# Performance work log

Measured on AMD Instinct MI355X. Metric: run time of the kernel, lower is better.

The kernel has to match this reference:

```python
import jax, jax.numpy as jnp
import numpy as np

B_IN, C, K, P, STRIDE, ITERS = 32, 32, 3, 4, 2, 3
PSIZE = P * P


def _patch(t):
    # t: (b, h, w, B, d) -> (b, oh, ow, K, K, B, d), matching torch fancy-index patching
    b, h, w = t.shape[:3]
    oh = int((h - K + 1) / STRIDE)
    idx = (np.arange(oh) * STRIDE)[:, None] + np.arange(K)[None, :]  # (oh, K)
    t = t[:, idx]          # (b, oh, K, w, B, d)
    t = t[:, :, :, idx]    # (b, oh, K, ow, K, B, d)
    perm = (0, 1, 3, 2, 4) + tuple(range(5, t.ndim))
    return jnp.transpose(t, perm), oh, oh


def _forward(x, a, weights, beta_u, beta_a):
    b = x.shape[0]
    KKB = K * K * B_IN
    p_in, oh, ow = _patch(x)
    a_in, _, _ = _patch(a)
    pose = p_in.reshape(b, oh, ow, KKB, P, P)
    a_in = a_in.reshape(b, oh, ow, KKB, 1)
    # voting: per-capsule 4x4 matmul with transformation matrices
    v = jnp.einsum('bhwnij,ncjl->bhwncil', pose, weights).reshape(b, oh, ow, KKB, C, PSIZE)
    eps = 1e-6
    lam = 1e-3
    ln2pi = np.float32(np.log(2.0 * np.pi))
    mu = sigma_sq = a_out = None
    for it in range(ITERS):
        if it == 0:
            r = jnp.full((b, oh, ow, KKB, C), 1.0 / C, jnp.float32) * a_in  # a_in broadcasts over C
        else:
            # gaussian log-likelihood of each vote under each output capsule
            ln_pjh = -(v - mu) ** 2 / (2.0 * sigma_sq) - 0.5 * jnp.log(sigma_sq) - 0.5 * ln2pi
            ln_ap = ln_pjh.sum(axis=5) + jnp.log(a_out.reshape(b, oh, ow, 1, C))
            r = jax.nn.softmax(ln_ap, axis=4)
        r_sum = r.sum(axis=3, keepdims=True)               # (b,oh,ow,1,C)
        coeff = (r / (r_sum + eps))[..., None]             # (b,oh,ow,KKB,C,1)
        mu = (coeff * v).sum(axis=3, keepdims=True)        # (b,oh,ow,1,C,PSIZE)
        sigma_sq = (coeff * (v - mu) ** 2).sum(axis=3, keepdims=True) + eps
        # beta_u: (C,1) broadcasts against (...,C,PSIZE); log(sqrt(s)) == 0.5*log(s)
        cost_h = (beta_u + 0.5 * jnp.log(sigma_sq)) * r_sum[..., None]
        a_out = jax.nn.sigmoid(lam * (beta_a - cost_h.sum(axis=5, keepdims=True)))
    p_out = mu.reshape(b, oh, ow, C, PSIZE)
    a_out = a_out.reshape(b, oh, ow, C, 1)
    return p_out, a_out


def setup_inputs() -> dict:
    key = jax.random.key(0)
    k1, k2, k3, k4, k5 = jax.random.split(key, 5)
    x = jax.random.normal(k1, (8, 14, 14, B_IN, PSIZE), jnp.float32)
    a = jax.random.uniform(k2, (8, 14, 14, B_IN, 1), jnp.float32)
    weights = jax.random.normal(k3, (K * K * B_IN, C, P, P), jnp.float32)
    beta_u = jax.random.normal(k4, (C, 1), jnp.float32) * 0.1
    beta_a = jax.random.normal(k5, (C, 1), jnp.float32) * 0.1
    return {"x": x, "a": a, "weights": weights, "beta_u": beta_u, "beta_a": beta_a}


def reference(x, a, weights, beta_u, beta_a):
    return _forward(x, a, weights, beta_u, beta_a)
```

## Files before the change

kernel.cpp:

```cpp
#include <hip/hip_runtime.h>

#define APB 256
#define NPOS 288
#define NCH 6
#define CHUNK 48
#define PSTRIDE 1056


template<int IT>
__global__ __launch_bounds__(APB) void caps_acc(
    const float* __restrict__ xg,
    const float* __restrict__ ag,
    const float* __restrict__ wg,
    const float* __restrict__ bu,
    const float* __restrict__ ba,
    const float* __restrict__ pin,
    float* __restrict__ pout)
{
    __shared__ __align__(16) float pose_s[CHUNK * 16];
    __shared__ float a_s[CHUNK];
    __shared__ __align__(16) float scratch[4 * 32 * 33];
    __shared__ float rsum_part[4 * 32];
    __shared__ float mu_tab[512];
    __shared__ float i2s_tab[512];
    __shared__ float Kc_tab[32];

    const int tid = threadIdx.x;
    const int blk = blockIdx.x;
    const int pos = blk / NCH;
    const int ch  = blk - pos * NCH;
    const int bb  = pos / 36;
    const int rem = pos % 36;
    const int yy  = rem / 6;
    const int xx  = rem % 6;

    #pragma unroll
    for (int j = 0; j < 3; ++j) {
        const int e    = ch * 768 + j * 256 + tid;
        const int cell = e >> 9;
        const int off  = e & 511;
        const int kh = cell / 3, kw = cell % 3;
        pose_s[j * 256 + tid] =
            xg[(size_t)((((bb * 14) + (2 * yy + kh)) * 14 + (2 * xx + kw)) * 32) * 16 + off];
    }
    if (IT == 0) {
        if (tid < CHUNK) {
            const int e    = ch * CHUNK + tid;
            const int cell = e >> 5;
            const int bi   = e & 31;
            const int kh = cell / 3, kw = cell % 3;
            a_s[tid] = ag[(size_t)(((bb * 14) + (2 * yy + kh)) * 14 + (2 * xx + kw)) * 32 + bi];
        }
    }

    const int fc2 = tid >> 3;
    const int fh  = tid & 7;
    if (IT > 0) {
        const float* q0 = pin + (size_t)pos * (NCH * PSTRIDE) + fc2 * 33;
        float ms0 = 0.f, ms1 = 0.f, vs0 = 0.f, vs1 = 0.f, rsc = 0.f;
        #pragma unroll
        for (int cc = 0; cc < NCH; ++cc) {
            const float* q = q0 + cc * PSTRIDE;
            ms0 += q[fh];
            ms1 += q[fh + 8];
            vs0 += q[16 + fh];
            vs1 += q[16 + fh + 8];
            rsc += q[32];
        }
        const float inv  = 1.f / (rsc + 1e-6f);
        const float S    = rsc * inv;
        const float mu0  = ms0 * inv;
        const float mu1  = ms1 * inv;
        const float sig0 = vs0 * inv - mu0 * mu0 * (2.f - S) + 1e-6f;
        const float sig1 = vs1 * inv - mu1 * mu1 * (2.f - S) + 1e-6f;
        float lgs = __logf(sig0) + __logf(sig1);
        #pragma unroll
        for (int msk = 4; msk >= 1; msk >>= 1) lgs += __shfl_xor(lgs, msk);
        const float cost = rsc * (16.f * bu[fc2] + 0.5f * lgs);
        const float ao   = 1.f / (1.f + __expf(-0.001f * (ba[fc2] - cost)));
        mu_tab[fc2 * 16 + fh]      = mu0;
        mu_tab[fc2 * 16 + fh + 8]  = mu1;
        i2s_tab[fc2 * 16 + fh]     = 0.5f / sig0;
        i2s_tab[fc2 * 16 + fh + 8] = 0.5f / sig1;
        if (fh == 0) Kc_tab[fc2] = 0.5f * lgs - __logf(ao);
    }
    __syncthreads();

    const int c    = tid & 31;
    const int s    = tid >> 5;
    const int lane = tid & 63;
    const int wv   = tid >> 6;
    const float4* wp = (const float4*)wg;

    float mu_c[16], i2s_c[16], Kc = 0.f;
    if (IT > 0) {
        #pragma unroll
        for (int p = 0; p < 16; ++p) {
            mu_c[p]  = mu_tab[c * 16 + p];
            i2s_c[p] = i2s_tab[c * 16 + p];
        }
        Kc = Kc_tab[c];
    }
    float macc[16], vacc[16], rs = 0.f;
    #pragma unroll
    for (int p = 0; p < 16; ++p) { macc[p] = 0.f; vacc[p] = 0.f; }

    for (int k = 0; k < 6; ++k) {
        const int nl = s * 6 + k;
        const int n  = ch * CHUNK + nl;
        const float4* pp = (const float4*)&pose_s[nl << 4];
        float pf[16];
        float4 q;
        q = pp[0]; pf[0]=q.x;  pf[1]=q.y;  pf[2]=q.z;  pf[3]=q.w;
        q = pp[1]; pf[4]=q.x;  pf[5]=q.y;  pf[6]=q.z;  pf[7]=q.w;
        q = pp[2]; pf[8]=q.x;  pf[9]=q.y;  pf[10]=q.z; pf[11]=q.w;
        q = pp[3]; pf[12]=q.x; pf[13]=q.y; pf[14]=q.z; pf[15]=q.w;
        const int wbase = (n * 32 + c) * 4;
        float v[16];
        #pragma unroll
        for (int p = 0; p < 16; ++p) v[p] = 0.f;
        #pragma unroll
        for (int j = 0; j < 4; ++j) {
            const float4 w = wp[wbase + j];
            #pragma unroll
            for (int i = 0; i < 4; ++i) {
                const float pj = pf[i * 4 + j];
                v[i*4+0] = fmaf(pj, w.x, v[i*4+0]);
                v[i*4+1] = fmaf(pj, w.y, v[i*4+1]);
                v[i*4+2] = fmaf(pj, w.z, v[i*4+2]);
                v[i*4+3] = fmaf(pj, w.w, v[i*4+3]);
            }
        }
        float r;
        if (IT == 0) {
            r = a_s[nl] * 0.03125f;
        } else {
            float t0 = 0.f, t1 = 0.f, t2 = 0.f, t3 = 0.f;
            #pragma unroll
            for (int p = 0; p < 16; p += 4) {
                float d0 = v[p]   - mu_c[p];   t0 = fmaf(d0*d0, i2s_c[p],   t0);
                float d1 = v[p+1] - mu_c[p+1]; t1 = fmaf(d1*d1, i2s_c[p+1], t1);
                float d2 = v[p+2] - mu_c[p+2]; t2 = fmaf(d2*d2, i2s_c[p+2], t2);
                float d3 = v[p+3] - mu_c[p+3]; t3 = fmaf(d3*d3, i2s_c[p+3], t3);
            }
            float lnap = -((t0 + t1) + (t2 + t3)) - Kc;
            float m = lnap;
            #pragma unroll
            for (int msk = 16; msk >= 1; msk >>= 1) m = fmaxf(m, __shfl_xor(m, msk));
            float e = __expf(lnap - m);
            float sum = e;
            #pragma unroll
            for (int msk = 16; msk >= 1; msk >>= 1) sum += __shfl_xor(sum, msk);
            r = e / sum;
        }
        rs += r;
        #pragma unroll
        for (int p = 0; p < 16; ++p) {
            float rv = r * v[p];
            macc[p] += rv;
            vacc[p] = fmaf(rv, v[p], vacc[p]);
        }
    }

    #pragma unroll
    for (int p = 0; p < 16; ++p) {
        macc[p] += __shfl_xor(macc[p], 32);
        vacc[p] += __shfl_xor(vacc[p], 32);
    }
    rs += __shfl_xor(rs, 32);
    if (lane < 32) {
        const int base = (wv * 32 + lane) * 33;
        #pragma unroll
        for (int p = 0; p < 16; ++p) {
            scratch[base + p]      = macc[p];
            scratch[base + 16 + p] = vacc[p];
        }
        rsum_part[wv * 32 + lane] = rs;
    }
    __syncthreads();

    float ms0 = 0.f, ms1 = 0.f, vs0 = 0.f, vs1 = 0.f, rsc = 0.f;
    #pragma unroll
    for (int w = 0; w < 4; ++w) {
        const int base = (w * 32 + fc2) * 33;
        ms0 += scratch[base + fh];
        ms1 += scratch[base + fh + 8];
        vs0 += scratch[base + 16 + fh];
        vs1 += scratch[base + 16 + fh + 8];
        rsc += rsum_part[w * 32 + fc2];
    }
    float* po = pout + (size_t)(pos * NCH + ch) * PSTRIDE + fc2 * 33;
    po[fh]          = ms0;
    po[fh + 8]      = ms1;
    po[16 + fh]     = vs0;
    po[16 + fh + 8] = vs1;
    if (fh == 0) po[32] = rsc;
}

__global__ __launch_bounds__(512) void caps_fin(
    const float* __restrict__ pin,
    const float* __restrict__ bu,
    const float* __restrict__ ba,
    float* __restrict__ outp)
{
    const int tid = threadIdx.x;
    const int pos = blockIdx.x;
    const int fc = tid >> 4, fp = tid & 15;
    const float* q0 = pin + (size_t)pos * (NCH * PSTRIDE) + fc * 33;
    float ms = 0.f, vs = 0.f, rsc = 0.f;
    #pragma unroll
    for (int cc = 0; cc < NCH; ++cc) {
        const float* q = q0 + cc * PSTRIDE;
        ms  += q[fp];
        vs  += q[16 + fp];
        rsc += q[32];
    }
    const float inv = 1.f / (rsc + 1e-6f);
    const float S   = rsc * inv;
    const float mu  = ms * inv;
    const float sig = vs * inv - mu * mu * (2.f - S) + 1e-6f;
    const float lg  = __logf(sig);
    float lgs = lg;
    #pragma unroll
    for (int msk = 8; msk >= 1; msk >>= 1) lgs += __shfl_xor(lgs, msk);
    const float cost = rsc * (16.f * bu[fc] + 0.5f * lgs);
    const float ao   = 1.f / (1.f + __expf(-0.001f * (ba[fc] - cost)));
    outp[(size_t)pos * 512 + tid] = mu;
    if (fp == 0) outp[147456 + (size_t)pos * 32 + fc] = ao;
}

__global__ __launch_bounds__(512) void convcaps_kernel(
    const float* __restrict__ xg,
    const float* __restrict__ ag,
    const float* __restrict__ wg,
    const float* __restrict__ bu,
    const float* __restrict__ ba,
    float* __restrict__ outp)
{
    __shared__ __align__(16) float pose_s[4608];
    __shared__ float a_s[288];
    __shared__ __align__(16) float scratch[8448];
    __shared__ float rsum_part[256];
    __shared__ float mu_tab[512];
    __shared__ float i2s_tab[512];
    __shared__ float aout_tab[32];
    __shared__ float Kc_tab[32];

    const int tid = threadIdx.x;
    const int pos = blockIdx.x;
    const int bb  = pos / 36;
    const int rem = pos % 36;
    const int yy  = rem / 6;
    const int xx  = rem % 6;

    #pragma unroll
    for (int wi = 0; wi < 9; ++wi) {
        const int kh = wi / 3, kw = wi % 3;
        const float* src =
            xg + (size_t)((((bb * 14) + (2 * yy + kh)) * 14 + (2 * xx + kw)) * 32) * 16;
        pose_s[wi * 512 + tid] = src[tid];
    }
    if (tid < 288) {
        const int wi = tid >> 5, bi = tid & 31;
        const int kh = wi / 3, kw = wi % 3;
        a_s[tid] = ag[(size_t)(((bb * 14) + (2 * yy + kh)) * 14 + (2 * xx + kw)) * 32 + bi];
    }
    __syncthreads();

    const int c    = tid & 31;
    const int s    = tid >> 5;
    const int lane = tid & 63;
    const int wv   = tid >> 6;
    const float4* wp = (const float4*)wg;

    for (int it = 0; it < 3; ++it) {
        float mu_c[16], i2s_c[16], Kc = 0.f;
        if (it > 0) {
            #pragma unroll
            for (int p = 0; p < 16; ++p) {
                mu_c[p]  = mu_tab[c * 16 + p];
                i2s_c[p] = i2s_tab[c * 16 + p];
            }
            Kc = Kc_tab[c];
        }
        float macc[16], vacc[16], rs = 0.f;
        #pragma unroll
        for (int p = 0; p < 16; ++p) { macc[p] = 0.f; vacc[p] = 0.f; }

        for (int k = 0; k < 18; ++k) {
            const int n = s * 18 + k;
            const float4* pp = (const float4*)&pose_s[n << 4];
            float pf[16];
            float4 q;
            q = pp[0]; pf[0]=q.x; pf[1]=q.y; pf[2]=q.z;  pf[3]=q.w;
            q = pp[1]; pf[4]=q.x; pf[5]=q.y; pf[6]=q.z;  pf[7]=q.w;
            q = pp[2]; pf[8]=q.x; pf[9]=q.y; pf[10]=q.z; pf[11]=q.w;
            q = pp[3]; pf[12]=q.x; pf[13]=q.y; pf[14]=q.z; pf[15]=q.w;
            const int wbase = (n * 32 + c) * 4;
            float v[16];
            #pragma unroll
            for (int p = 0; p < 16; ++p) v[p] = 0.f;
            #pragma unroll
            for (int j = 0; j < 4; ++j) {
                const float4 w = wp[wbase + j];
                #pragma unroll
                for (int i = 0; i < 4; ++i) {
                    const float pj = pf[i * 4 + j];
                    v[i*4+0] = fmaf(pj, w.x, v[i*4+0]);
                    v[i*4+1] = fmaf(pj, w.y, v[i*4+1]);
                    v[i*4+2] = fmaf(pj, w.z, v[i*4+2]);
                    v[i*4+3] = fmaf(pj, w.w, v[i*4+3]);
                }
            }
            float r;
            if (it == 0) {
                r = a_s[n] * 0.03125f;
            } else {
                float t = 0.f;
                #pragma unroll
                for (int p = 0; p < 16; ++p) {
                    float d = v[p] - mu_c[p];
                    t = fmaf(d * d, i2s_c[p], t);
                }
                float lnap = -t - Kc;
                float m = lnap;
                #pragma unroll
                for (int msk = 16; msk >= 1; msk >>= 1) m = fmaxf(m, __shfl_xor(m, msk));
                float e = __expf(lnap - m);
                float sum = e;
                #pragma unroll
                for (int msk = 16; msk >= 1; msk >>= 1) sum += __shfl_xor(sum, msk);
                r = e / sum;
            }
            rs += r;
            #pragma unroll
            for (int p = 0; p < 16; ++p) {
                float rv = r * v[p];
                macc[p] += rv;
                vacc[p] = fmaf(rv, v[p], vacc[p]);
            }
        }

        #pragma unroll
        for (int p = 0; p < 16; ++p) {
            macc[p] += __shfl_xor(macc[p], 32);
            vacc[p] += __shfl_xor(vacc[p], 32);
        }
        rs += __shfl_xor(rs, 32);
        if (lane < 32) {
            const int base = (wv * 32 + lane) * 33;
            #pragma unroll
            for (int p = 0; p < 16; ++p) {
                scratch[base + p]      = macc[p];
                scratch[base + 16 + p] = vacc[p];
            }
            rsum_part[wv * 32 + lane] = rs;
        }
        __syncthreads();

        const int fc = tid >> 4, fp = tid & 15;
        float ms = 0.f, vs = 0.f, rsc = 0.f;
        #pragma unroll
        for (int w = 0; w < 8; ++w) {
            ms  += scratch[(w * 32 + fc) * 33 + fp];
            vs  += scratch[(w * 32 + fc) * 33 + 16 + fp];
            rsc += rsum_part[w * 32 + fc];
        }
        const float inv = 1.f / (rsc + 1e-6f);
        const float S   = rsc * inv;
        const float mu  = ms * inv;
        const float sig = vs * inv - mu * mu * (2.f - S) + 1e-6f;
        const float lg  = __logf(sig);
        float lgs = lg;
        #pragma unroll
        for (int msk = 8; msk >= 1; msk >>= 1) lgs += __shfl_xor(lgs, msk);
        const float buv  = bu[fc];
        const float bav  = ba[fc];
        const float cost = rsc * (16.f * buv + 0.5f * lgs);
        const float ao   = 1.f / (1.f + __expf(-0.001f * (bav - cost)));

        mu_tab[fc * 16 + fp]  = mu;
        i2s_tab[fc * 16 + fp] = 0.5f / sig;
        if (fp == 0) {
            aout_tab[fc] = ao;
            Kc_tab[fc]   = 0.5f * lgs - __logf(ao);
        }

        if (it == 2) {
            outp[(size_t)pos * 512 + tid] = mu;
            if (fp == 0) outp[147456 + (size_t)pos * 32 + fc] = ao;
        }
        __syncthreads();
    }
}

extern "C" void kernel_launch(void* const* d_in, const int* in_sizes, int n_in,
                              void* d_out, int out_size, void* d_ws, size_t ws_size,
                              hipStream_t stream) {
    (void)in_sizes; (void)n_in; (void)out_size;
    const float* x  = (const float*)d_in[0];
    const float* a  = (const float*)d_in[1];
    const float* w  = (const float*)d_in[2];
    const float* bu = (const float*)d_in[3];
    const float* ba = (const float*)d_in[4];
    float* out = (float*)d_out;

    const size_t buf_elems = (size_t)NPOS * NCH * PSTRIDE;
    if (ws_size < 2 * buf_elems * sizeof(float)) {
        convcaps_kernel<<<dim3(288), dim3(512), 0, stream>>>(x, a, w, bu, ba, out);
        return;
    }
    float* buf0 = (float*)d_ws;
    float* buf1 = buf0 + buf_elems;

    caps_acc<0><<<dim3(NPOS * NCH), dim3(APB), 0, stream>>>(x, a, w, bu, ba, nullptr, buf0);
    caps_acc<1><<<dim3(NPOS * NCH), dim3(APB), 0, stream>>>(x, a, w, bu, ba, buf0, buf1);
    caps_acc<2><<<dim3(NPOS * NCH), dim3(APB), 0, stream>>>(x, a, w, bu, ba, buf1, buf0);
    caps_fin<<<dim3(NPOS), dim3(512), 0, stream>>>(buf0, bu, ba, out);
}
```

Baseline: 142.5 us.

## Fuse final reduction into last EM pass and streamline E-step math

Removes the separate finalize kernel by having the last of the six chunk blocks per position, found through an atomic counter, compute mu and the activations. It expands the Gaussian exponent into precomputed a·v², b·v and constant tables, and uses DPP lane moves for the 32-lane softmax reductions. It also prefetches the next weight matrix in registers, pads the per-capsule partial layout so loads and stores are float4, and uses a fast divide. The counter fusion adds threadfence and atomic overhead, and the algebraic expansion may lose some precision.

```diff
diff --git a/kernel.cpp b/kernel.cpp
--- a/kernel.cpp
+++ b/kernel.cpp
@@ -1,29 +1,84 @@
 #include <hip/hip_runtime.h>
 
-#define APB 256
 #define NPOS 288
 #define NCH 6
 #define CHUNK 48
-#define PSTRIDE 1056
-
+#define CSTRIDE 36
+#define PSTRIDE (32 * CSTRIDE)
+
+template<int CTRL>
+__device__ __forceinline__ float dpp_mov(float x) {
+    return __int_as_float(__builtin_amdgcn_update_dpp(
+        0, __float_as_int(x), CTRL, 0xF, 0xF, true));
+}
+__device__ __forceinline__ float red32_max(float x) {
+    x = fmaxf(x, dpp_mov<0x121>(x));
+    x = fmaxf(x, dpp_mov<0x122>(x));
+    x = fmaxf(x, dpp_mov<0x124>(x));
+    x = fmaxf(x, dpp_mov<0x128>(x));
+    return fmaxf(x, __shfl_xor(x, 16));
+}
+__device__ __forceinline__ float red32_sum(float x) {
+    x += dpp_mov<0x121>(x);
+    x += dpp_mov<0x122>(x);
+    x += dpp_mov<0x124>(x);
+    x += dpp_mov<0x128>(x);
+    return x + __shfl_xor(x, 16);
+}
+
+#define DOT4(pa, c0, c1, c2, c3) fmaf(pa.x, c0, fmaf(pa.y, c1, fmaf(pa.z, c2, pa.w * c3)))
+#define VROWS() \
+    v0.x = DOT4(pa0, wa0.x, wa1.x, wa2.x, wa3.x); \
+    v0.y = DOT4(pa0, wa0.y, wa1.y, wa2.y, wa3.y); \
+    v0.z = DOT4(pa0, wa0.z, wa1.z, wa2.z, wa3.z); \
+    v0.w = DOT4(pa0, wa0.w, wa1.w, wa2.w, wa3.w); \
+    v1.x = DOT4(pa1, wa0.x, wa1.x, wa2.x, wa3.x); \
+    v1.y = DOT4(pa1, wa0.y, wa1.y, wa2.y, wa3.y); \
+    v1.z = DOT4(pa1, wa0.z, wa1.z, wa2.z, wa3.z); \
+    v1.w = DOT4(pa1, wa0.w, wa1.w, wa2.w, wa3.w); \
+    v2.x = DOT4(pa2, wa0.x, wa1.x, wa2.x, wa3.x); \
+    v2.y = DOT4(pa2, wa0.y, wa1.y, wa2.y, wa3.y); \
+    v2.z = DOT4(pa2, wa0.z, wa1.z, wa2.z, wa3.z); \
+    v2.w = DOT4(pa2, wa0.w, wa1.w, wa2.w, wa3.w); \
+    v3.x = DOT4(pa3, wa0.x, wa1.x, wa2.x, wa3.x); \
+    v3.y = DOT4(pa3, wa0.y, wa1.y, wa2.y, wa3.y); \
+    v3.z = DOT4(pa3, wa0.z, wa1.z, wa2.z, wa3.z); \
+    v3.w = DOT4(pa3, wa0.w, wa1.w, wa2.w, wa3.w);
+#define SQ4(d, v) d.x = v.x*v.x; d.y = v.y*v.y; d.z = v.z*v.z; d.w = v.w*v.w;
+#define TU4(t, u, v, q, A, B) \
+    t = fmaf(q.x, A.x, t); u = fmaf(v.x, B.x, u); \
+    t = fmaf(q.y, A.y, t); u = fmaf(v.y, B.y, u); \
+    t = fmaf(q.z, A.z, t); u = fmaf(v.z, B.z, u); \
+    t = fmaf(q.w, A.w, t); u = fmaf(v.w, B.w, u);
+#define RACC(mai, vai, vi, qi) \
+    mai.x = fmaf(r, vi.x, mai.x); vai.x = fmaf(r, qi.x, vai.x); \
+    mai.y = fmaf(r, vi.y, mai.y); vai.y = fmaf(r, qi.y, vai.y); \
+    mai.z = fmaf(r, vi.z, mai.z); vai.z = fmaf(r, qi.z, vai.z); \
+    mai.w = fmaf(r, vi.w, mai.w); vai.w = fmaf(r, qi.w, vai.w);
+#define XRED(vi) \
+    vi.x += __shfl_xor(vi.x, 32); vi.y += __shfl_xor(vi.y, 32); \
+    vi.z += __shfl_xor(vi.z, 32); vi.w += __shfl_xor(vi.w, 32);
 
 template<int IT>
-__global__ __launch_bounds__(APB) void caps_acc(
+__global__ __launch_bounds__(256) void caps_acc(
     const float* __restrict__ xg,
     const float* __restrict__ ag,
     const float* __restrict__ wg,
     const float* __restrict__ bu,
     const float* __restrict__ ba,
     const float* __restrict__ pin,
-    float* __restrict__ pout)
+    float* __restrict__ pout,
+    float* __restrict__ outg,
+    unsigned* __restrict__ cnt)
 {
     __shared__ __align__(16) float pose_s[CHUNK * 16];
     __shared__ float a_s[CHUNK];
     __shared__ __align__(16) float scratch[4 * 32 * 33];
     __shared__ float rsum_part[4 * 32];
-    __shared__ float mu_tab[512];
     __shared__ float i2s_tab[512];
-    __shared__ float Kc_tab[32];
+    __shared__ float b_tab[512];
+    __shared__ float c_tab[32];
+    __shared__ int   last_s;
 
     const int tid = threadIdx.x;
     const int blk = blockIdx.x;
@@ -51,38 +106,43 @@
             const int kh = cell / 3, kw = cell % 3;
             a_s[tid] = ag[(size_t)(((bb * 14) + (2 * yy + kh)) * 14 + (2 * xx + kw)) * 32 + bi];
         }
+        if (ch == 0 && tid == 0) cnt[pos] = 0u;
     }
 
     const int fc2 = tid >> 3;
     const int fh  = tid & 7;
     if (IT > 0) {
-        const float* q0 = pin + (size_t)pos * (NCH * PSTRIDE) + fc2 * 33;
+        const float* q0 = pin + (size_t)pos * (NCH * PSTRIDE) + fc2 * CSTRIDE;
         float ms0 = 0.f, ms1 = 0.f, vs0 = 0.f, vs1 = 0.f, rsc = 0.f;
         #pragma unroll
         for (int cc = 0; cc < NCH; ++cc) {
             const float* q = q0 + cc * PSTRIDE;
-            ms0 += q[fh];
-            ms1 += q[fh + 8];
-            vs0 += q[16 + fh];
-            vs1 += q[16 + fh + 8];
+            const float4 m4 = *(const float4*)&q[fh * 4];
+            ms0 += m4.x; ms1 += m4.y; vs0 += m4.z; vs1 += m4.w;
             rsc += q[32];
         }
         const float inv  = 1.f / (rsc + 1e-6f);
         const float S    = rsc * inv;
-        const float mu0  = ms0 * inv;
-        const float mu1  = ms1 * inv;
-        const float sig0 = vs0 * inv - mu0 * mu0 * (2.f - S) + 1e-6f;
-        const float sig1 = vs1 * inv - mu1 * mu1 * (2.f - S) + 1e-6f;
-        float lgs = __logf(sig0) + __logf(sig1);
-        #pragma unroll
-        for (int msk = 4; msk >= 1; msk >>= 1) lgs += __shfl_xor(lgs, msk);
+        const float mmu0 = ms0 * inv;
+        const float mmu1 = ms1 * inv;
+        const float sg0  = vs0 * inv - mmu0 * mmu0 * (2.f - S) + 1e-6f;
+        const float sg1  = vs1 * inv - mmu1 * mmu1 * (2.f - S) + 1e-6f;
+        const float i0   = 0.5f / sg0;
+        const float i1   = 0.5f / sg1;
+        float lgs = __logf(sg0) + __logf(sg1);
+        float m2  = fmaf(mmu0 * mmu0, i0, mmu1 * mmu1 * i1);
+        #pragma unroll
+        for (int msk = 4; msk >= 1; msk >>= 1) {
+            lgs += __shfl_xor(lgs, msk);
+            m2  += __shfl_xor(m2, msk);
+        }
         const float cost = rsc * (16.f * bu[fc2] + 0.5f * lgs);
         const float ao   = 1.f / (1.f + __expf(-0.001f * (ba[fc2] - cost)));
-        mu_tab[fc2 * 16 + fh]      = mu0;
-        mu_tab[fc2 * 16 + fh + 8]  = mu1;
-        i2s_tab[fc2 * 16 + fh]     = 0.5f / sig0;
-        i2s_tab[fc2 * 16 + fh + 8] = 0.5f / sig1;
-        if (fh == 0) Kc_tab[fc2] = 0.5f * lgs - __logf(ao);
+        i2s_tab[fc2 * 16 + fh]     = i0;
+        i2s_tab[fc2 * 16 + fh + 8] = i1;
+        b_tab[fc2 * 16 + fh]       = mmu0 * i0;
+        b_tab[fc2 * 16 + fh + 8]   = mmu1 * i1;
+        if (fh == 0) c_tab[fc2] = m2 + 0.5f * lgs - __logf(ao);
     }
     __syncthreads();
 
@@ -92,89 +152,81 @@
     const int wv   = tid >> 6;
     const float4* wp = (const float4*)wg;
 
-    float mu_c[16], i2s_c[16], Kc = 0.f;
+    float4 A0, A1, A2, A3, B0, B1, B2, B3;
+    float C = 0.f;
     if (IT > 0) {
-        #pragma unroll
-        for (int p = 0; p < 16; ++p) {
-            mu_c[p]  = mu_tab[c * 16 + p];
-            i2s_c[p] = i2s_tab[c * 16 + p];
-        }
-        Kc = Kc_tab[c];
-    }
-    float macc[16], vacc[16], rs = 0.f;
-    #pragma unroll
-    for (int p = 0; p < 16; ++p) { macc[p] = 0.f; vacc[p] = 0.f; }
-
-    for (int k = 0; k < 6; ++k) {
-        const int nl = s * 6 + k;
-        const int n  = ch * CHUNK + nl;
-        const float4* pp = (const float4*)&pose_s[nl << 4];
-        float pf[16];
-        float4 q;
-        q = pp[0]; pf[0]=q.x;  pf[1]=q.y;  pf[2]=q.z;  pf[3]=q.w;
-        q = pp[1]; pf[4]=q.x;  pf[5]=q.y;  pf[6]=q.z;  pf[7]=q.w;
-        q = pp[2]; pf[8]=q.x;  pf[9]=q.y;  pf[10]=q.z; pf[11]=q.w;
-        q = pp[3]; pf[12]=q.x; pf[13]=q.y; pf[14]=q.z; pf[15]=q.w;
-        const int wbase = (n * 32 + c) * 4;
-        float v[16];
-        #pragma unroll
-        for (int p = 0; p < 16; ++p) v[p] = 0.f;
-        #pragma unroll
-        for (int j = 0; j < 4; ++j) {
-            const float4 w = wp[wbase + j];
-            #pragma unroll
-            for (int i = 0; i < 4; ++i) {
-                const float pj = pf[i * 4 + j];
-                v[i*4+0] = fmaf(pj, w.x, v[i*4+0]);
-                v[i*4+1] = fmaf(pj, w.y, v[i*4+1]);
-                v[i*4+2] = fmaf(pj, w.z, v[i*4+2]);
-                v[i*4+3] = fmaf(pj, w.w, v[i*4+3]);
-            }
-        }
-        float r;
-        if (IT == 0) {
-            r = a_s[nl] * 0.03125f;
-        } else {
-            float t0 = 0.f, t1 = 0.f, t2 = 0.f, t3 = 0.f;
-            #pragma unroll
-            for (int p = 0; p < 16; p += 4) {
-                float d0 = v[p]   - mu_c[p];   t0 = fmaf(d0*d0, i2s_c[p],   t0);
-                float d1 = v[p+1] - mu_c[p+1]; t1 = fmaf(d1*d1, i2s_c[p+1], t1);
-                float d2 = v[p+2] - mu_c[p+2]; t2 = fmaf(d2*d2, i2s_c[p+2], t2);
-                float d3 = v[p+3] - mu_c[p+3]; t3 = fmaf(d3*d3, i2s_c[p+3], t3);
-            }
-            float lnap = -((t0 + t1) + (t2 + t3)) - Kc;
-            float m = lnap;
-            #pragma unroll
-            for (int msk = 16; msk >= 1; msk >>= 1) m = fmaxf(m, __shfl_xor(m, msk));
-            float e = __expf(lnap - m);
-            float sum = e;
-            #pragma unroll
-            for (int msk = 16; msk >= 1; msk >>= 1) sum += __shfl_xor(sum, msk);
-            r = e / sum;
-        }
-        rs += r;
-        #pragma unroll
-        for (int p = 0; p < 16; ++p) {
-            float rv = r * v[p];
-            macc[p] += rv;
-            vacc[p] = fmaf(rv, v[p], vacc[p]);
-        }
-    }
-
-    #pragma unroll
-    for (int p = 0; p < 16; ++p) {
-        macc[p] += __shfl_xor(macc[p], 32);
-        vacc[p] += __shfl_xor(vacc[p], 32);
-    }
+        A0 = *(const float4*)&i2s_tab[c * 16 + 0];
+        A1 = *(const float4*)&i2s_tab[c * 16 + 4];
+        A2 = *(const float4*)&i2s_tab[c * 16 + 8];
+        A3 = *(const float4*)&i2s_tab[c * 16 + 12];
+        B0 = *(const float4*)&b_tab[c * 16 + 0];
+        B1 = *(const float4*)&b_tab[c * 16 + 4];
+        B2 = *(const float4*)&b_tab[c * 16 + 8];
+        B3 = *(const float4*)&b_tab[c * 16 + 12];
+        C  = c_tab[c];
+    }
+
+    float4 ma0, ma1, ma2, ma3, va0, va1, va2, va3;
+    ma0 = ma1 = ma2 = ma3 = make_float4(0.f, 0.f, 0.f, 0.f);
+    va0 = va1 = va2 = va3 = make_float4(0.f, 0.f, 0.f, 0.f);
+    float rs = 0.f;
+
+    const int n0 = ch * CHUNK + s * 6;
+    const float4* wptr = wp + (size_t)(n0 * 32 + c) * 4;
+    float4 wa0 = wptr[0], wa1 = wptr[1], wa2 = wptr[2], wa3 = wptr[3];
+
+    #define EM_STEP_ACC(NL)                                                \
+    {                                                                      \
+        const float4* pp = (const float4*)&pose_s[(NL) << 4];              \
+        float4 pa0 = pp[0], pa1 = pp[1], pa2 = pp[2], pa3 = pp[3];         \
+        float4 v0, v1, v2, v3;                                             \
+        VROWS()                                                            \
+        float4 q0_, q1_, q2_, q3_;                                         \
+        SQ4(q0_, v0) SQ4(q1_, v1) SQ4(q2_, v2) SQ4(q3_, v3)                \
+        float r;                                                           \
+        if (IT == 0) {                                                     \
+            r = a_s[NL] * 0.03125f;                                        \
+        } else {                                                           \
+            float t01 = 0.f, u01 = 0.f, t23 = 0.f, u23 = 0.f;              \
+            TU4(t01, u01, v0, q0_, A0, B0)                                 \
+            TU4(t01, u01, v1, q1_, A1, B1)                                 \
+            TU4(t23, u23, v2, q2_, A2, B2)                                 \
+            TU4(t23, u23, v3, q3_, A3, B3)                                 \
+            const float lnap = fmaf(2.f, u01 + u23, -(t01 + t23)) - C;     \
+            const float m    = red32_max(lnap);                            \
+            const float e    = __expf(lnap - m);                           \
+            const float sum  = red32_sum(e);                               \
+            r = __fdividef(e, sum);                                        \
+        }                                                                  \
+        rs += r;                                                           \
+        RACC(ma0, va0, v0, q0_)                                            \
+        RACC(ma1, va1, v1, q1_)                                            \
+        RACC(ma2, va2, v2, q2_)                                            \
+        RACC(ma3, va3, v3, q3_)                                            \
+    }
+
+    for (int k = 0; k < 5; ++k) {
+        const float4* wnext = wptr + 128;
+        float4 wn0 = wnext[0], wn1 = wnext[1], wn2 = wnext[2], wn3 = wnext[3];
+        EM_STEP_ACC(s * 6 + k)
+        wa0 = wn0; wa1 = wn1; wa2 = wn2; wa3 = wn3; wptr = wnext;
+    }
+    EM_STEP_ACC(s * 6 + 5)
+    #undef EM_STEP_ACC
+
+    XRED(ma0) XRED(ma1) XRED(ma2) XRED(ma3)
+    XRED(va0) XRED(va1) XRED(va2) XRED(va3)
     rs += __shfl_xor(rs, 32);
     if (lane < 32) {
         const int base = (wv * 32 + lane) * 33;
-        #pragma unroll
-        for (int p = 0; p < 16; ++p) {
-            scratch[base + p]      = macc[p];
-            scratch[base + 16 + p] = vacc[p];
-        }
+        scratch[base+0]=ma0.x;  scratch[base+1]=ma0.y;  scratch[base+2]=ma0.z;  scratch[base+3]=ma0.w;
+        scratch[base+4]=ma1.x;  scratch[base+5]=ma1.y;  scratch[base+6]=ma1.z;  scratch[base+7]=ma1.w;
+        scratch[base+8]=ma2.x;  scratch[base+9]=ma2.y;  scratch[base+10]=ma2.z; scratch[base+11]=ma2.w;
+        scratch[base+12]=ma3.x; scratch[base+13]=ma3.y; scratch[base+14]=ma3.z; scratch[base+15]=ma3.w;
+        scratch[base+16]=va0.x; scratch[base+17]=va0.y; scratch[base+18]=va0.z; scratch[base+19]=va0.w;
+        scratch[base+20]=va1.x; scratch[base+21]=va1.y; scratch[base+22]=va1.z; scratch[base+23]=va1.w;
+        scratch[base+24]=va2.x; scratch[base+25]=va2.y; scratch[base+26]=va2.z; scratch[base+27]=va2.w;
+        scratch[base+28]=va3.x; scratch[base+29]=va3.y; scratch[base+30]=va3.z; scratch[base+31]=va3.w;
         rsum_part[wv * 32 + lane] = rs;
     }
     __syncthreads();
@@ -189,44 +241,44 @@
         vs1 += scratch[base + 16 + fh + 8];
         rsc += rsum_part[w * 32 + fc2];
     }
-    float* po = pout + (size_t)(pos * NCH + ch) * PSTRIDE + fc2 * 33;
-    po[fh]          = ms0;
-    po[fh + 8]      = ms1;
-    po[16 + fh]     = vs0;
-    po[16 + fh + 8] = vs1;
+    float* po = pout + (size_t)(pos * NCH + ch) * PSTRIDE + fc2 * CSTRIDE;
+    *(float4*)&po[fh * 4] = make_float4(ms0, ms1, vs0, vs1);
     if (fh == 0) po[32] = rsc;
-}
-
-__global__ __launch_bounds__(512) void caps_fin(
-    const float* __restrict__ pin,
-    const float* __restrict__ bu,
-    const float* __restrict__ ba,
-    float* __restrict__ outp)
-{
-    const int tid = threadIdx.x;
-    const int pos = blockIdx.x;
-    const int fc = tid >> 4, fp = tid & 15;
-    const float* q0 = pin + (size_t)pos * (NCH * PSTRIDE) + fc * 33;
-    float ms = 0.f, vs = 0.f, rsc = 0.f;
-    #pragma unroll
-    for (int cc = 0; cc < NCH; ++cc) {
-        const float* q = q0 + cc * PSTRIDE;
-        ms  += q[fp];
-        vs  += q[16 + fp];
-        rsc += q[32];
-    }
-    const float inv = 1.f / (rsc + 1e-6f);
-    const float S   = rsc * inv;
-    const float mu  = ms * inv;
-    const float sig = vs * inv - mu * mu * (2.f - S) + 1e-6f;
-    const float lg  = __logf(sig);
-    float lgs = lg;
-    #pragma unroll
-    for (int msk = 8; msk >= 1; msk >>= 1) lgs += __shfl_xor(lgs, msk);
-    const float cost = rsc * (16.f * bu[fc] + 0.5f * lgs);
-    const float ao   = 1.f / (1.f + __expf(-0.001f * (ba[fc] - cost)));
-    outp[(size_t)pos * 512 + tid] = mu;
-    if (fp == 0) outp[147456 + (size_t)pos * 32 + fc] = ao;
+
+    if (IT == 2) {
+        __threadfence();
+        __syncthreads();
+        if (tid == 0) last_s = (atomicAdd(&cnt[pos], 1u) == NCH - 1u);
+        __syncthreads();
+        if (last_s) {
+            __threadfence();
+            const int fp = tid & 15;
+            #pragma unroll
+            for (int half = 0; half < 2; ++half) {
+                const int fc = (tid >> 4) + half * 16;
+                const float* qq = pout + (size_t)pos * (NCH * PSTRIDE) + fc * CSTRIDE;
+                float ms = 0.f, vs = 0.f, rc = 0.f;
+                #pragma unroll
+                for (int cc = 0; cc < NCH; ++cc) {
+                    const float* q = qq + cc * PSTRIDE;
+                    ms += q[(fp & 7) * 4 + (fp >> 3)];
+                    vs += q[(fp & 7) * 4 + 2 + (fp >> 3)];
+                    rc += q[32];
+                }
+                const float inv = 1.f / (rc + 1e-6f);
+                const float S   = rc * inv;
+                const float mu  = ms * inv;
+                const float sig = vs * inv - mu * mu * (2.f - S) + 1e-6f;
+                float lgs = __logf(sig);
+                #pragma unroll
+                for (int msk = 8; msk >= 1; msk >>= 1) lgs += __shfl_xor(lgs, msk);
+                const float cost = rc * (16.f * bu[fc] + 0.5f * lgs);
+                const float ao   = 1.f / (1.f + __expf(-0.001f * (ba[fc] - cost)));
+                outg[(size_t)pos * 512 + fc * 16 + fp] = mu;
+                if (fp == 0) outg[147456 + (size_t)pos * 32 + fc] = ao;
+            }
+        }
+    }
 }
 
 __global__ __launch_bounds__(512) void convcaps_kernel(
@@ -243,7 +295,6 @@
     __shared__ float rsum_part[256];
     __shared__ float mu_tab[512];
     __shared__ float i2s_tab[512];
-    __shared__ float aout_tab[32];
     __shared__ float Kc_tab[32];
 
     const int tid = threadIdx.x;
@@ -370,21 +421,15 @@
         const float S   = rsc * inv;
         const float mu  = ms * inv;
         const float sig = vs * inv - mu * mu * (2.f - S) + 1e-6f;
-        const float lg  = __logf(sig);
-        float lgs = lg;
+        float lgs = __logf(sig);
         #pragma unroll
         for (int msk = 8; msk >= 1; msk >>= 1) lgs += __shfl_xor(lgs, msk);
-        const float buv  = bu[fc];
-        const float bav  = ba[fc];
-        const float cost = rsc * (16.f * buv + 0.5f * lgs);
-        const float ao   = 1.f / (1.f + __expf(-0.001f * (bav - cost)));
+        const float cost = rsc * (16.f * bu[fc] + 0.5f * lgs);
+        const float ao   = 1.f / (1.f + __expf(-0.001f * (ba[fc] - cost)));
 
         mu_tab[fc * 16 + fp]  = mu;
         i2s_tab[fc * 16 + fp] = 0.5f / sig;
-        if (fp == 0) {
-            aout_tab[fc] = ao;
-            Kc_tab[fc]   = 0.5f * lgs - __logf(ao);
-        }
+        if (fp == 0) Kc_tab[fc] = 0.5f * lgs - __logf(ao);
 
         if (it == 2) {
             outp[(size_t)pos * 512 + tid] = mu;
@@ -406,15 +451,16 @@
     float* out = (float*)d_out;
 
     const size_t buf_elems = (size_t)NPOS * NCH * PSTRIDE;
-    if (ws_size < 2 * buf_elems * sizeof(float)) {
+    const size_t need = (2 * buf_elems) * sizeof(float) + NPOS * sizeof(unsigned);
+    if (ws_size < need) {
         convcaps_kernel<<<dim3(288), dim3(512), 0, stream>>>(x, a, w, bu, ba, out);
         return;
     }
     float* buf0 = (float*)d_ws;
     float* buf1 = buf0 + buf_elems;
-
-    caps_acc<0><<<dim3(NPOS * NCH), dim3(APB), 0, stream>>>(x, a, w, bu, ba, nullptr, buf0);
-    caps_acc<1><<<dim3(NPOS * NCH), dim3(APB), 0, stream>>>(x, a, w, bu, ba, buf0, buf1);
-    caps_acc<2><<<dim3(NPOS * NCH), dim3(APB), 0, stream>>>(x, a, w, bu, ba, buf1, buf0);
-    caps_fin<<<dim3(NPOS), dim3(512), 0, stream>>>(buf0, bu, ba, out);
-}
+    unsigned* cnt = (unsigned*)(buf0 + 2 * buf_elems);
+
+    caps_acc<0><<<dim3(NPOS * NCH), dim3(256), 0, stream>>>(x, a, w, bu, ba, nullptr, buf0, out, cnt);
+    caps_acc<1><<<dim3(NPOS * NCH), dim3(256), 0, stream>>>(x, a, w, bu, ba, buf0, buf1, out, cnt);
+    caps_acc<2><<<dim3(NPOS * NCH), dim3(256), 0, stream>>>(x, a, w, bu, ba, buf1, buf0, out, cnt);
+}
```

Result: slower. 399.4 us (+180.2%).
